# Optimization experiments

Measured on AMD Instinct MI355X. Metric: run time of the kernel, lower is better.

## Reference

```python
import jax, jax.numpy as jnp
import numpy as np

H = 1024
V = 32000
L = 4096


def setup_inputs() -> dict:
    key = jax.random.key(0)
    ks = jax.random.split(key, 20)
    s = 1.0 / np.sqrt(H)
    d = {}
    d["input_token"] = jax.random.randint(ks[0], (1,), 0, V)
    d["hidden"] = jax.random.normal(ks[1], (1, 1, H), jnp.float32)
    d["encoder_hiddens"] = jax.random.normal(ks[2], (L, H), jnp.float32)
    # parameters
    d["emb"] = jax.random.normal(ks[3], (V, H), jnp.float32)
    d["wW"] = jax.random.uniform(ks[4], (H, H), jnp.float32, -s, s)
    d["wb"] = jax.random.uniform(ks[5], (H,), jnp.float32, -s, s)
    d["uW"] = jax.random.uniform(ks[6], (H, H), jnp.float32, -s, s)
    d["ub"] = jax.random.uniform(ks[7], (H,), jnp.float32, -s, s)
    d["vW"] = jax.random.uniform(ks[8], (1, H), jnp.float32, -s, s)
    d["cW"] = jax.random.uniform(ks[9], (H, 2 * H), jnp.float32, -s, s)
    d["cb"] = jax.random.uniform(ks[10], (H,), jnp.float32, -s, s)
    d["w_ih"] = jax.random.uniform(ks[11], (3 * H, H), jnp.float32, -s, s)
    d["b_ih"] = jax.random.uniform(ks[12], (3 * H,), jnp.float32, -s, s)
    d["w_hh"] = jax.random.uniform(ks[13], (3 * H, H), jnp.float32, -s, s)
    d["b_hh"] = jax.random.uniform(ks[14], (3 * H,), jnp.float32, -s, s)
    d["outW"] = jax.random.uniform(ks[15], (V, H), jnp.float32, -s, s)
    d["outb"] = jax.random.uniform(ks[16], (V,), jnp.float32, -s, s)
    return d


def reference(input_token, hidden, encoder_hiddens, emb, wW, wb, uW, ub, vW,
              cW, cb, w_ih, b_ih, w_hh, b_hh, outW, outb):
    # embedding lookup, dropout is identity (p=0 / eval)
    embedded = emb[input_token[0]]  # [H]
    # additive attention: w(hidden[0]) + u(enc) -> tanh -> v -> softmax
    h0 = hidden[0]  # [1, H] (first/only layer)
    scores = jnp.tanh(h0 @ wW.T + wb + encoder_hiddens @ uW.T + ub) @ vW[0]  # [L]
    attn_weights = jax.nn.softmax(scores, axis=-1)  # [L]
    context = attn_weights @ encoder_hiddens  # [H]
    # combine + relu
    x = jnp.concatenate([context, embedded])  # [2H]
    x = jax.nn.relu(x @ cW.T + cb)  # [H]
    # single GRU cell step (torch GRU gate order: r, z, n)
    hprev = hidden[0, 0]  # [H]
    gi = x @ w_ih.T + b_ih
    gh = hprev @ w_hh.T + b_hh
    ir, iz, inn = jnp.split(gi, 3)
    hr, hz, hn = jnp.split(gh, 3)
    r = jax.nn.sigmoid(ir + hr)
    z = jax.nn.sigmoid(iz + hz)
    n = jnp.tanh(inn + r * hn)
    hnew = (1.0 - z) * n + z * hprev  # [H]
    new_hidden = hnew.reshape(1, 1, H)
    # residual + output projection
    out = (context.reshape(1, 1, H) + new_hidden)
    logits = out @ outW.T + outb  # [1, 1, V]
    return logits, new_hidden, attn_weights
```

## Files before the change

### kernel.cpp

```cpp
#include <hip/hip_runtime.h>
#include <hip/hip_bf16.h>
#include <math.h>

#define H 1024
#define V 32000
#define L 4096

typedef __bf16 bf16x8 __attribute__((ext_vector_type(8)));
typedef float f32x4 __attribute__((ext_vector_type(4)));

__device__ __forceinline__ unsigned short f32_to_bf16(float f) {
    unsigned int u = __float_as_uint(f);
    unsigned int r = (u + 0x7fffu + ((u >> 16) & 1u)) >> 16;
    return (unsigned short)r;
}

__device__ __forceinline__ float dot4(float4 a, float4 b) {
    return a.x * b.x + a.y * b.y + a.z * b.z + a.w * b.w;
}

__device__ __forceinline__ float wave_reduce(float v) {
    for (int off = 32; off; off >>= 1) v += __shfl_xor(v, off);
    return v;
}

__global__ __launch_bounds__(256) void prep_wh_kernel(
        const float* __restrict__ enc,
        const float* __restrict__ uW,
        const float* __restrict__ emb,
        const int* __restrict__ token,
        const float* __restrict__ h0,
        const float* __restrict__ wW,
        const float* __restrict__ wb,
        const float* __restrict__ ub,
        unsigned short* __restrict__ enc_bf,
        unsigned short* __restrict__ u_bf,
        float* __restrict__ emb_vec,
        float* __restrict__ wh) {
    if (blockIdx.x < 1024) {
        int tid = blockIdx.x * 256 + threadIdx.x;
        const int stride = 1024 * 256;
        const int NE = L * H / 4;
        const int NU = H * H / 4;
        for (int i = tid; i < NE; i += stride) {
            float4 f = ((const float4*)enc)[i];
            ushort4 o;
            o.x = f32_to_bf16(f.x); o.y = f32_to_bf16(f.y);
            o.z = f32_to_bf16(f.z); o.w = f32_to_bf16(f.w);
            ((ushort4*)enc_bf)[i] = o;
        }
        for (int i = tid; i < NU; i += stride) {
            float4 f = ((const float4*)uW)[i];
            ushort4 o;
            o.x = f32_to_bf16(f.x); o.y = f32_to_bf16(f.y);
            o.z = f32_to_bf16(f.z); o.w = f32_to_bf16(f.w);
            ((ushort4*)u_bf)[i] = o;
        }
        int t0 = token[0];
        for (int i = tid; i < H; i += stride) emb_vec[i] = emb[(size_t)t0 * H + i];
    } else {
        int wave = ((blockIdx.x - 1024) * 256 + threadIdx.x) >> 6;
        int lane = threadIdx.x & 63;
        const float4* row = (const float4*)(wW + (size_t)wave * H);
        const float4* hv = (const float4*)h0;
        float acc = 0.f;
#pragma unroll
        for (int i = 0; i < 4; i++) {
            int idx = i * 64 + lane;
            acc += dot4(row[idx], hv[idx]);
        }
        acc = wave_reduce(acc);
        if (lane == 0) wh[wave] = acc + wb[wave] + ub[wave];
    }
}

#define APITCH 72
__global__ __launch_bounds__(256) void scores_kernel(
        const unsigned short* __restrict__ enc_bf,
        const unsigned short* __restrict__ u_bf,
        const float* __restrict__ wh,
        const float* __restrict__ vW,
        float* __restrict__ scores_part) {
    __shared__ unsigned short Als[32 * APITCH];
    __shared__ unsigned short Bls[128 * APITCH];
    int tid = threadIdx.x;
    int wave = tid >> 6, lane = tid & 63;
    int wm = wave >> 1, wn = wave & 1;
    int mrow = lane & 15, quad = lane >> 4;
    int r0b = blockIdx.x * 32;
    int jc0b = blockIdx.y * 128;

    f32x4 acc[4];
#pragma unroll
    for (int i = 0; i < 4; i++) acc[i] = (f32x4){0.f, 0.f, 0.f, 0.f};

    for (int k0 = 0; k0 < H; k0 += 64) {
        {
            int row = tid >> 3, ko = (tid & 7) * 8;
            uint4 v = *(const uint4*)(enc_bf + (size_t)(r0b + row) * H + k0 + ko);
            *(uint4*)(Als + row * APITCH + ko) = v;
        }
#pragma unroll
        for (int c = 0; c < 4; c++) {
            int chunk = c * 256 + tid;
            int j = chunk >> 3, ko = (chunk & 7) * 8;
            uint4 v = *(const uint4*)(u_bf + (size_t)(jc0b + j) * H + k0 + ko);
            *(uint4*)(Bls + j * APITCH + ko) = v;
        }
        __syncthreads();

        const unsigned short* abase = Als + (wm * 16 + mrow) * APITCH + quad * 8;
        bf16x8 a0 = *(const bf16x8*)(abase);
        bf16x8 a1 = *(const bf16x8*)(abase + 32);
#pragma unroll
        for (int jt = 0; jt < 4; jt++) {
            const unsigned short* bbase =
                Bls + (wn * 64 + jt * 16 + mrow) * APITCH + quad * 8;
            bf16x8 b0 = *(const bf16x8*)(bbase);
            bf16x8 b1 = *(const bf16x8*)(bbase + 32);
            acc[jt] = __builtin_amdgcn_mfma_f32_16x16x32_bf16(a0, b0, acc[jt], 0, 0, 0);
            acc[jt] = __builtin_amdgcn_mfma_f32_16x16x32_bf16(a1, b1, acc[jt], 0, 0, 0);
        }
        __syncthreads();
    }

    float sacc[4] = {0.f, 0.f, 0.f, 0.f};
#pragma unroll
    for (int jt = 0; jt < 4; jt++) {
        int jcol = jc0b + wn * 64 + jt * 16 + mrow;
        float vj = vW[jcol];
        float whv = wh[jcol];
#pragma unroll
        for (int r = 0; r < 4; r++) {
            sacc[r] += vj * tanhf(acc[jt][r] + whv);
        }
    }
#pragma unroll
    for (int r = 0; r < 4; r++) {
        float s = sacc[r];
        s += __shfl_xor(s, 1);
        s += __shfl_xor(s, 2);
        s += __shfl_xor(s, 4);
        s += __shfl_xor(s, 8);
        if (mrow == 0)
            scores_part[(blockIdx.y * 2 + wn) * L + r0b + wm * 16 + quad * 4 + r] = s;
    }
}

__global__ __launch_bounds__(1024) void softmax_kernel(
        const float* __restrict__ scores_part,
        float* __restrict__ attn_ws,
        float* __restrict__ attn_out,
        float* __restrict__ context) {
    __shared__ float smax[16];
    __shared__ float ssum[16];
    int tid = threadIdx.x;
    int wid = tid >> 6, lane = tid & 63;
    context[tid] = 0.f;
    float4 sv = ((const float4*)scores_part)[tid];
#pragma unroll
    for (int c = 1; c < 16; c++) {
        float4 p = ((const float4*)(scores_part + c * L))[tid];
        sv.x += p.x; sv.y += p.y; sv.z += p.z; sv.w += p.w;
    }
    float vmax = fmaxf(fmaxf(sv.x, sv.y), fmaxf(sv.z, sv.w));
    for (int off = 32; off; off >>= 1) vmax = fmaxf(vmax, __shfl_xor(vmax, off));
    if (lane == 0) smax[wid] = vmax;
    __syncthreads();
    if (tid == 0) {
        float m = smax[0];
        for (int i = 1; i < 16; i++) m = fmaxf(m, smax[i]);
        smax[0] = m;
    }
    __syncthreads();
    float gmax = smax[0];
    float e0 = expf(sv.x - gmax), e1 = expf(sv.y - gmax);
    float e2 = expf(sv.z - gmax), e3 = expf(sv.w - gmax);
    float s = e0 + e1 + e2 + e3;
    s = wave_reduce(s);
    if (lane == 0) ssum[wid] = s;
    __syncthreads();
    if (tid == 0) {
        float t = 0.f;
        for (int i = 0; i < 16; i++) t += ssum[i];
        ssum[0] = t;
    }
    __syncthreads();
    float inv = 1.0f / ssum[0];
    float4 o = make_float4(e0 * inv, e1 * inv, e2 * inv, e3 * inv);
    ((float4*)attn_ws)[tid] = o;
    ((float4*)attn_out)[tid] = o;
}

__global__ void context_kernel(const float* __restrict__ enc,
                               const float* __restrict__ attn,
                               float* __restrict__ context) {
    int col = blockIdx.x * 256 + threadIdx.x;
    int l0 = blockIdx.y * 32;
    float acc = 0.f;
    for (int l = l0; l < l0 + 32; l++) acc += attn[l] * enc[(size_t)l * H + col];
    atomicAdd(&context[col], acc);
}

__global__ void combine_kernel(const float* __restrict__ context,
                               const float* __restrict__ emb_vec,
                               const float* __restrict__ cW,
                               const float* __restrict__ cb,
                               float* __restrict__ xvec) {
    int wave = (blockIdx.x * blockDim.x + threadIdx.x) >> 6;
    int lane = threadIdx.x & 63;
    if (wave >= H) return;
    const float4* row = (const float4*)(cW + (size_t)wave * 2 * H);
    const float4* cv = (const float4*)context;
    const float4* ev = (const float4*)emb_vec;
    float acc = 0.f;
#pragma unroll
    for (int i = 0; i < 4; i++) {
        int idx = i * 64 + lane;
        acc += dot4(row[idx], cv[idx]);
        acc += dot4(row[256 + idx], ev[idx]);
    }
    acc = wave_reduce(acc);
    if (lane == 0) xvec[wave] = fmaxf(acc + cb[wave], 0.f);
}

__global__ void gru_kernel(const float* __restrict__ xvec,
                           const float* __restrict__ hprev,
                           const float* __restrict__ w_ih,
                           const float* __restrict__ b_ih,
                           const float* __restrict__ w_hh,
                           const float* __restrict__ b_hh,
                           const float* __restrict__ context,
                           float* __restrict__ hnew_out,
                           float* __restrict__ ovec) {
    int j = (blockIdx.x * blockDim.x + threadIdx.x) >> 6;
    int lane = threadIdx.x & 63;
    if (j >= H) return;
    const float4* xv = (const float4*)xvec;
    const float4* hv = (const float4*)hprev;
    float a0 = 0.f, a1 = 0.f, a2 = 0.f, a3 = 0.f, a4 = 0.f, a5 = 0.f;
#pragma unroll
    for (int i = 0; i < 4; i++) {
        int idx = i * 64 + lane;
        float4 x4 = xv[idx], h4 = hv[idx];
        a0 += dot4(((const float4*)(w_ih + (size_t)j * H))[idx], x4);
        a1 += dot4(((const float4*)(w_ih + (size_t)(H + j) * H))[idx], x4);
        a2 += dot4(((const float4*)(w_ih + (size_t)(2 * H + j) * H))[idx], x4);
        a3 += dot4(((const float4*)(w_hh + (size_t)j * H))[idx], h4);
        a4 += dot4(((const float4*)(w_hh + (size_t)(H + j) * H))[idx], h4);
        a5 += dot4(((const float4*)(w_hh + (size_t)(2 * H + j) * H))[idx], h4);
    }
    a0 = wave_reduce(a0); a1 = wave_reduce(a1); a2 = wave_reduce(a2);
    a3 = wave_reduce(a3); a4 = wave_reduce(a4); a5 = wave_reduce(a5);
    if (lane == 0) {
        float ir = a0 + b_ih[j], iz = a1 + b_ih[H + j], inn = a2 + b_ih[2 * H + j];
        float hr = a3 + b_hh[j], hz = a4 + b_hh[H + j], hn = a5 + b_hh[2 * H + j];
        float r = 1.f / (1.f + expf(-(ir + hr)));
        float z = 1.f / (1.f + expf(-(iz + hz)));
        float n = tanhf(inn + r * hn);
        float hp = hprev[j];
        float hval = (1.f - z) * n + z * hp;
        hnew_out[j] = hval;
        ovec[j] = context[j] + hval;
    }
}

__global__ __launch_bounds__(256) void logits_kernel(
        const float* __restrict__ ovec,
        const float* __restrict__ outW,
        const float* __restrict__ outb,
        float* __restrict__ out) {
    int wave = (blockIdx.x * blockDim.x + threadIdx.x) >> 6;
    int lane = threadIdx.x & 63;
    int i0 = wave * 2;
    if (i0 >= V) return;
    const float4* row0 = (const float4*)(outW + (size_t)i0 * H);
    const float4* row1 = (const float4*)(outW + (size_t)(i0 + 1) * H);
    const float4* ov = (const float4*)ovec;
    float acc0 = 0.f, acc1 = 0.f;
#pragma unroll
    for (int t = 0; t < 4; t++) {
        int idx = t * 64 + lane;
        float4 o4 = ov[idx];
        acc0 += dot4(row0[idx], o4);
        acc1 += dot4(row1[idx], o4);
    }
    acc0 = wave_reduce(acc0);
    acc1 = wave_reduce(acc1);
    if (lane == 0) {
        out[i0] = acc0 + outb[i0];
        out[i0 + 1] = acc1 + outb[i0 + 1];
    }
}

extern "C" void kernel_launch(void* const* d_in, const int* in_sizes, int n_in,
                              void* d_out, int out_size, void* d_ws, size_t ws_size,
                              hipStream_t stream) {
    const int* token = (const int*)d_in[0];
    const float* hidden = (const float*)d_in[1];
    const float* enc = (const float*)d_in[2];
    const float* emb = (const float*)d_in[3];
    const float* wW = (const float*)d_in[4];
    const float* wb = (const float*)d_in[5];
    const float* uW = (const float*)d_in[6];
    const float* ub = (const float*)d_in[7];
    const float* vW = (const float*)d_in[8];
    const float* cW = (const float*)d_in[9];
    const float* cb = (const float*)d_in[10];
    const float* w_ih = (const float*)d_in[11];
    const float* b_ih = (const float*)d_in[12];
    const float* w_hh = (const float*)d_in[13];
    const float* b_hh = (const float*)d_in[14];
    const float* outW = (const float*)d_in[15];
    const float* outb = (const float*)d_in[16];
    float* out = (float*)d_out;

    char* ws = (char*)d_ws;
    unsigned short* enc_bf = (unsigned short*)ws;
    unsigned short* u_bf = (unsigned short*)(ws + (size_t)L * H * 2);
    float* whv = (float*)(ws + (size_t)L * H * 2 + (size_t)H * H * 2);
    float* emb_vec = whv + H;
    float* scores_part = emb_vec + H;
    float* attn = scores_part + 16 * L;
    float* context = attn + L;
    float* xvec = context + H;
    float* ovec = xvec + H;

    prep_wh_kernel<<<1280, 256, 0, stream>>>(enc, uW, emb, token, hidden, wW, wb, ub,
                                             enc_bf, u_bf, emb_vec, whv);
    scores_kernel<<<dim3(128, 8), 256, 0, stream>>>(enc_bf, u_bf, whv, vW, scores_part);
    softmax_kernel<<<1, 1024, 0, stream>>>(scores_part, attn, out + V + H, context);
    context_kernel<<<dim3(4, 128), 256, 0, stream>>>(enc, attn, context);
    combine_kernel<<<256, 256, 0, stream>>>(context, emb_vec, cW, cb, xvec);
    gru_kernel<<<256, 256, 0, stream>>>(xvec, hidden, w_ih, b_ih, w_hh, b_hh,
                                        context, out + V, ovec);
    logits_kernel<<<4000, 256, 0, stream>>>(ovec, outW, outb, out);
}
```

Baseline: 355.8 us.

## Fuse softmax into context kernel, atomic score accumulation, larger M tile

New measurement: 343.2 us. 3.5% less time.

```diff
diff --git a/kernel.cpp b/kernel.cpp
--- a/kernel.cpp
+++ b/kernel.cpp
@@ -36,7 +36,8 @@
         unsigned short* __restrict__ enc_bf,
         unsigned short* __restrict__ u_bf,
         float* __restrict__ emb_vec,
-        float* __restrict__ wh) {
+        float* __restrict__ wh,
+        float* __restrict__ scores) {
     if (blockIdx.x < 1024) {
         int tid = blockIdx.x * 256 + threadIdx.x;
         const int stride = 1024 * 256;
@@ -59,6 +60,8 @@
         int t0 = token[0];
         for (int i = tid; i < H; i += stride) emb_vec[i] = emb[(size_t)t0 * H + i];
     } else {
+        int z = (blockIdx.x - 1024) * 256 + threadIdx.x;
+        if (z < L) scores[z] = 0.f;
         int wave = ((blockIdx.x - 1024) * 256 + threadIdx.x) >> 6;
         int lane = threadIdx.x & 63;
         const float4* row = (const float4*)(wW + (size_t)wave * H);
@@ -80,125 +83,146 @@
         const unsigned short* __restrict__ u_bf,
         const float* __restrict__ wh,
         const float* __restrict__ vW,
-        float* __restrict__ scores_part) {
-    __shared__ unsigned short Als[32 * APITCH];
+        float* __restrict__ scores,
+        float* __restrict__ context) {
+    __shared__ unsigned short Als[64 * APITCH];
     __shared__ unsigned short Bls[128 * APITCH];
     int tid = threadIdx.x;
+    if (blockIdx.x == 0 && blockIdx.y == 0) {
+        ((float4*)context)[tid] = make_float4(0.f, 0.f, 0.f, 0.f);
+    }
     int wave = tid >> 6, lane = tid & 63;
     int wm = wave >> 1, wn = wave & 1;
     int mrow = lane & 15, quad = lane >> 4;
-    int r0b = blockIdx.x * 32;
+    int r0b = blockIdx.x * 64;
     int jc0b = blockIdx.y * 128;
 
-    f32x4 acc[4];
-#pragma unroll
-    for (int i = 0; i < 4; i++) acc[i] = (f32x4){0.f, 0.f, 0.f, 0.f};
+    f32x4 acc[2][4];
+#pragma unroll
+    for (int mt = 0; mt < 2; mt++)
+#pragma unroll
+        for (int jt = 0; jt < 4; jt++) acc[mt][jt] = (f32x4){0.f, 0.f, 0.f, 0.f};
 
     for (int k0 = 0; k0 < H; k0 += 64) {
-        {
-            int row = tid >> 3, ko = (tid & 7) * 8;
-            uint4 v = *(const uint4*)(enc_bf + (size_t)(r0b + row) * H + k0 + ko);
-            *(uint4*)(Als + row * APITCH + ko) = v;
+#pragma unroll
+        for (int c = 0; c < 2; c++) {
+            int chunk = c * 256 + tid;
+            int row = chunk >> 3, ko = (chunk & 7) * 8;
+            *(uint4*)(Als + row * APITCH + ko) =
+                *(const uint4*)(enc_bf + (size_t)(r0b + row) * H + k0 + ko);
         }
 #pragma unroll
         for (int c = 0; c < 4; c++) {
             int chunk = c * 256 + tid;
             int j = chunk >> 3, ko = (chunk & 7) * 8;
-            uint4 v = *(const uint4*)(u_bf + (size_t)(jc0b + j) * H + k0 + ko);
-            *(uint4*)(Bls + j * APITCH + ko) = v;
+            *(uint4*)(Bls + j * APITCH + ko) =
+                *(const uint4*)(u_bf + (size_t)(jc0b + j) * H + k0 + ko);
         }
         __syncthreads();
 
-        const unsigned short* abase = Als + (wm * 16 + mrow) * APITCH + quad * 8;
-        bf16x8 a0 = *(const bf16x8*)(abase);
-        bf16x8 a1 = *(const bf16x8*)(abase + 32);
+        bf16x8 a[2][2];
+#pragma unroll
+        for (int mt = 0; mt < 2; mt++) {
+            const unsigned short* abase =
+                Als + (wm * 32 + mt * 16 + mrow) * APITCH + quad * 8;
+            a[mt][0] = *(const bf16x8*)(abase);
+            a[mt][1] = *(const bf16x8*)(abase + 32);
+        }
 #pragma unroll
         for (int jt = 0; jt < 4; jt++) {
             const unsigned short* bbase =
                 Bls + (wn * 64 + jt * 16 + mrow) * APITCH + quad * 8;
             bf16x8 b0 = *(const bf16x8*)(bbase);
             bf16x8 b1 = *(const bf16x8*)(bbase + 32);
-            acc[jt] = __builtin_amdgcn_mfma_f32_16x16x32_bf16(a0, b0, acc[jt], 0, 0, 0);
-            acc[jt] = __builtin_amdgcn_mfma_f32_16x16x32_bf16(a1, b1, acc[jt], 0, 0, 0);
+#pragma unroll
+            for (int mt = 0; mt < 2; mt++) {
+                acc[mt][jt] = __builtin_amdgcn_mfma_f32_16x16x32_bf16(a[mt][0], b0, acc[mt][jt], 0, 0, 0);
+                acc[mt][jt] = __builtin_amdgcn_mfma_f32_16x16x32_bf16(a[mt][1], b1, acc[mt][jt], 0, 0, 0);
+            }
         }
         __syncthreads();
     }
 
-    float sacc[4] = {0.f, 0.f, 0.f, 0.f};
+    float sacc[2][4] = {{0.f, 0.f, 0.f, 0.f}, {0.f, 0.f, 0.f, 0.f}};
 #pragma unroll
     for (int jt = 0; jt < 4; jt++) {
         int jcol = jc0b + wn * 64 + jt * 16 + mrow;
         float vj = vW[jcol];
         float whv = wh[jcol];
 #pragma unroll
+        for (int mt = 0; mt < 2; mt++)
+#pragma unroll
+            for (int r = 0; r < 4; r++)
+                sacc[mt][r] += vj * tanhf(acc[mt][jt][r] + whv);
+    }
+#pragma unroll
+    for (int mt = 0; mt < 2; mt++)
+#pragma unroll
         for (int r = 0; r < 4; r++) {
-            sacc[r] += vj * tanhf(acc[jt][r] + whv);
-        }
-    }
-#pragma unroll
-    for (int r = 0; r < 4; r++) {
-        float s = sacc[r];
-        s += __shfl_xor(s, 1);
-        s += __shfl_xor(s, 2);
-        s += __shfl_xor(s, 4);
-        s += __shfl_xor(s, 8);
-        if (mrow == 0)
-            scores_part[(blockIdx.y * 2 + wn) * L + r0b + wm * 16 + quad * 4 + r] = s;
-    }
-}
-
-__global__ __launch_bounds__(1024) void softmax_kernel(
-        const float* __restrict__ scores_part,
-        float* __restrict__ attn_ws,
-        float* __restrict__ attn_out,
-        float* __restrict__ context) {
-    __shared__ float smax[16];
-    __shared__ float ssum[16];
+            float s = sacc[mt][r];
+            s += __shfl_xor(s, 1);
+            s += __shfl_xor(s, 2);
+            s += __shfl_xor(s, 4);
+            s += __shfl_xor(s, 8);
+            if (mrow == 0)
+                atomicAdd(&scores[r0b + wm * 32 + mt * 16 + quad * 4 + r], s);
+        }
+}
+
+__global__ __launch_bounds__(256) void ctx_softmax_kernel(
+        const float* __restrict__ scores,
+        const float* __restrict__ enc,
+        float* __restrict__ context,
+        float* __restrict__ attn_out) {
+    __shared__ float smax[4];
+    __shared__ float ssum[4];
+    __shared__ float attn_l[32];
     int tid = threadIdx.x;
     int wid = tid >> 6, lane = tid & 63;
-    context[tid] = 0.f;
-    float4 sv = ((const float4*)scores_part)[tid];
-#pragma unroll
-    for (int c = 1; c < 16; c++) {
-        float4 p = ((const float4*)(scores_part + c * L))[tid];
-        sv.x += p.x; sv.y += p.y; sv.z += p.z; sv.w += p.w;
-    }
-    float vmax = fmaxf(fmaxf(sv.x, sv.y), fmaxf(sv.z, sv.w));
-    for (int off = 32; off; off >>= 1) vmax = fmaxf(vmax, __shfl_xor(vmax, off));
-    if (lane == 0) smax[wid] = vmax;
+    float4 s0 = ((const float4*)scores)[tid];
+    float4 s1 = ((const float4*)scores)[256 + tid];
+    float4 s2 = ((const float4*)scores)[512 + tid];
+    float4 s3 = ((const float4*)scores)[768 + tid];
+    float m = fmaxf(fmaxf(fmaxf(s0.x, s0.y), fmaxf(s0.z, s0.w)),
+                    fmaxf(fmaxf(s1.x, s1.y), fmaxf(s1.z, s1.w)));
+    m = fmaxf(m, fmaxf(fmaxf(s2.x, s2.y), fmaxf(s2.z, s2.w)));
+    m = fmaxf(m, fmaxf(fmaxf(s3.x, s3.y), fmaxf(s3.z, s3.w)));
+    for (int off = 32; off; off >>= 1) m = fmaxf(m, __shfl_xor(m, off));
+    if (lane == 0) smax[wid] = m;
     __syncthreads();
-    if (tid == 0) {
-        float m = smax[0];
-        for (int i = 1; i < 16; i++) m = fmaxf(m, smax[i]);
-        smax[0] = m;
-    }
+    float gmax = fmaxf(fmaxf(smax[0], smax[1]), fmaxf(smax[2], smax[3]));
+    float e = expf(s0.x - gmax) + expf(s0.y - gmax) + expf(s0.z - gmax) + expf(s0.w - gmax)
+            + expf(s1.x - gmax) + expf(s1.y - gmax) + expf(s1.z - gmax) + expf(s1.w - gmax)
+            + expf(s2.x - gmax) + expf(s2.y - gmax) + expf(s2.z - gmax) + expf(s2.w - gmax)
+            + expf(s3.x - gmax) + expf(s3.y - gmax) + expf(s3.z - gmax) + expf(s3.w - gmax);
+    e = wave_reduce(e);
+    if (lane == 0) ssum[wid] = e;
     __syncthreads();
-    float gmax = smax[0];
-    float e0 = expf(sv.x - gmax), e1 = expf(sv.y - gmax);
-    float e2 = expf(sv.z - gmax), e3 = expf(sv.w - gmax);
-    float s = e0 + e1 + e2 + e3;
-    s = wave_reduce(s);
-    if (lane == 0) ssum[wid] = s;
+    float inv = 1.0f / (ssum[0] + ssum[1] + ssum[2] + ssum[3]);
+
+    int l0 = blockIdx.y * 32;
+    if (tid < 32) attn_l[tid] = expf(scores[l0 + tid] - gmax) * inv;
     __syncthreads();
-    if (tid == 0) {
-        float t = 0.f;
-        for (int i = 0; i < 16; i++) t += ssum[i];
-        ssum[0] = t;
-    }
-    __syncthreads();
-    float inv = 1.0f / ssum[0];
-    float4 o = make_float4(e0 * inv, e1 * inv, e2 * inv, e3 * inv);
-    ((float4*)attn_ws)[tid] = o;
-    ((float4*)attn_out)[tid] = o;
-}
-
-__global__ void context_kernel(const float* __restrict__ enc,
-                               const float* __restrict__ attn,
-                               float* __restrict__ context) {
-    int col = blockIdx.x * 256 + threadIdx.x;
-    int l0 = blockIdx.y * 32;
+
+    if (blockIdx.x == 0 && blockIdx.y == 0) {
+        float4 a0 = make_float4(expf(s0.x - gmax) * inv, expf(s0.y - gmax) * inv,
+                                expf(s0.z - gmax) * inv, expf(s0.w - gmax) * inv);
+        float4 a1 = make_float4(expf(s1.x - gmax) * inv, expf(s1.y - gmax) * inv,
+                                expf(s1.z - gmax) * inv, expf(s1.w - gmax) * inv);
+        float4 a2 = make_float4(expf(s2.x - gmax) * inv, expf(s2.y - gmax) * inv,
+                                expf(s2.z - gmax) * inv, expf(s2.w - gmax) * inv);
+        float4 a3 = make_float4(expf(s3.x - gmax) * inv, expf(s3.y - gmax) * inv,
+                                expf(s3.z - gmax) * inv, expf(s3.w - gmax) * inv);
+        ((float4*)attn_out)[tid] = a0;
+        ((float4*)attn_out)[256 + tid] = a1;
+        ((float4*)attn_out)[512 + tid] = a2;
+        ((float4*)attn_out)[768 + tid] = a3;
+    }
+
+    int col = blockIdx.x * 256 + tid;
     float acc = 0.f;
-    for (int l = l0; l < l0 + 32; l++) acc += attn[l] * enc[(size_t)l * H + col];
+#pragma unroll 4
+    for (int l = 0; l < 32; l++) acc += attn_l[l] * enc[(size_t)(l0 + l) * H + col];
     atomicAdd(&context[col], acc);
 }
 
@@ -320,17 +344,15 @@
     unsigned short* u_bf = (unsigned short*)(ws + (size_t)L * H * 2);
     float* whv = (float*)(ws + (size_t)L * H * 2 + (size_t)H * H * 2);
     float* emb_vec = whv + H;
-    float* scores_part = emb_vec + H;
-    float* attn = scores_part + 16 * L;
-    float* context = attn + L;
+    float* scores = emb_vec + H;
+    float* context = scores + L;
     float* xvec = context + H;
     float* ovec = xvec + H;
 
     prep_wh_kernel<<<1280, 256, 0, stream>>>(enc, uW, emb, token, hidden, wW, wb, ub,
-                                             enc_bf, u_bf, emb_vec, whv);
-    scores_kernel<<<dim3(128, 8), 256, 0, stream>>>(enc_bf, u_bf, whv, vW, scores_part);
-    softmax_kernel<<<1, 1024, 0, stream>>>(scores_part, attn, out + V + H, context);
-    context_kernel<<<dim3(4, 128), 256, 0, stream>>>(enc, attn, context);
+                                             enc_bf, u_bf, emb_vec, whv, scores);
+    scores_kernel<<<dim3(64, 8), 256, 0, stream>>>(enc_bf, u_bf, whv, vW, scores, context);
+    ctx_softmax_kernel<<<dim3(4, 128), 256, 0, stream>>>(scores, enc, context, out + V + H);
     combine_kernel<<<256, 256, 0, stream>>>(context, emb_vec, cW, cb, xvec);
     gru_kernel<<<256, 256, 0, stream>>>(xvec, hidden, w_ih, b_ih, w_hh, b_hh,
                                         context, out + V, ovec);
```
